# Performance work log

Measured on AMD Instinct MI355X. Metric: run time of the kernel, lower is better.

Reference implementation:

```python
import jax, jax.numpy as jnp
import numpy as np

SCALES = (3, 9, 17, 33)  # must be odd so padding=s//2 preserves spatial size


def _box_conv(img, s):
    # img: [B,1,H,W]; conv with an all-ones s x s kernel, 'same' padding for odd s
    k = jnp.ones((1, 1, s, s), img.dtype)
    p = s // 2
    return jax.lax.conv_general_dilated(
        img, k, window_strides=(1, 1), padding=[(p, p), (p, p)],
        dimension_numbers=("NCHW", "OIHW", "NCHW"))


def setup_inputs() -> dict:
    key = jax.random.key(0)
    B, C, H, W = 8, 3, 1024, 1024
    x = jax.random.normal(key, (B, C, H, W), dtype=jnp.float32)
    # mimicking sparse path-traced samples
    keep = jax.random.uniform(jax.random.fold_in(key, 1), (B, 1, H, W)) >= 0.3
    x = jnp.where(keep, x, 0.0)
    return {"x": x}


def reference(x):
    # F.conv2d(x, ones(1,3,1,1)/3) == per-pixel mean over the 3 channels
    lum = jnp.mean(x, axis=1, keepdims=True)          # [B,1,H,W]
    nonzero = (lum != 0).astype(lum.dtype)            # [B,1,H,W]
    feats = []
    for s in SCALES:
        count = _box_conv(nonzero, s)                 # number of nonzero pixels in window
        pool = _box_conv(lum, s) / jnp.maximum(count, 1.0)  # mean over nonzero pixels
        feats.append(count / float(s * s))            # percentage of nonzero pixels
        feats.append(pool)
    return jnp.concatenate(feats, axis=1)             # [B, 2*len(SCALES), H, W]
```

## Files before the change

kernel.cpp:

```cpp
#include <hip/hip_runtime.h>


constexpr int W_    = 1024;
constexpr int H_    = 1024;
constexpr int PAD   = 17;
constexpr int PROWS = H_ + 2 * PAD;
constexpr int LPAD  = 20;
constexpr int RW    = 1064;
constexpr int RS2   = 8;

template<int CTRL, int RM>
__device__ __forceinline__ int dppadd_i(int v) {
    int sh = __builtin_amdgcn_update_dpp(0, v, CTRL, RM, 0xF, true);
    return v + sh;
}

__device__ __forceinline__ int wave_iscan_i(int v) {
    v = dppadd_i<0x111, 0xF>(v);
    v = dppadd_i<0x112, 0xF>(v);
    v = dppadd_i<0x114, 0xF>(v);
    v = dppadd_i<0x118, 0xF>(v);
    v = dppadd_i<0x142, 0xA>(v);
    v = dppadd_i<0x143, 0xC>(v);
    return v;
}

__device__ __forceinline__ void ld4(const unsigned int* p, unsigned int r[4]) {
    __builtin_memcpy(r, p, 16);
}

__global__ __launch_bounds__(256)
void prefix_kernel(const float* __restrict__ x, unsigned int* __restrict__ P) {
    const int lane = threadIdx.x & 63;
    const int wv   = threadIdx.x >> 6;
    const int rp   = blockIdx.x * 4 + wv;
    const int b    = blockIdx.y;
    if (rp >= PROWS) return;

    unsigned int* prow = P + ((size_t)b * PROWS + rp) * RW;
    const int r = rp - PAD;

    if (r < 0 || r >= H_) {
        uint4 z = make_uint4(0u, 0u, 0u, 0u);
        for (int i = lane; i < RW / 4; i += 64)
            ((uint4*)prow)[i] = z;
        return;
    }

    const size_t HW = (size_t)H_ * W_;
    const float* px = x + (size_t)b * 3 * HW + (size_t)r * W_;

    int carry = 0;
    #pragma unroll
    for (int c = 0; c < 4; ++c) {
        const int col = c * 256 + 4 * lane;
        float4 r0 = *(const float4*)(px + col);
        float4 r1 = *(const float4*)(px + col + HW);
        float4 r2 = *(const float4*)(px + col + 2 * HW);
        float l0 = (r0.x + r1.x + r2.x) * (1.0f / 3.0f);
        float l1 = (r0.y + r1.y + r2.y) * (1.0f / 3.0f);
        float l2 = (r0.z + r1.z + r2.z) * (1.0f / 3.0f);
        float l3 = (r0.w + r1.w + r2.w) * (1.0f / 3.0f);
        int v0 = ((int)rintf(l0 * 1024.f) << 16) | ((l0 != 0.f) ? 1 : 0);
        int v1 = ((int)rintf(l1 * 1024.f) << 16) | ((l1 != 0.f) ? 1 : 0);
        int v2 = ((int)rintf(l2 * 1024.f) << 16) | ((l2 != 0.f) ? 1 : 0);
        int v3 = ((int)rintf(l3 * 1024.f) << 16) | ((l3 != 0.f) ? 1 : 0);
        int s0 = v0, s1 = s0 + v1, s2 = s1 + v2, s3 = s2 + v3;
        int incl = wave_iscan_i(s3);
        int excl = incl - s3 + carry;
        uint4 o = make_uint4((unsigned)(excl + s0), (unsigned)(excl + s1),
                             (unsigned)(excl + s2), (unsigned)(excl + s3));
        *(uint4*)(prow + LPAD + col) = o;
        carry += __shfl(incl, 63);
    }

    const unsigned int total = (unsigned int)carry;
    if (lane < 5) {
        *(uint4*)(prow + 4 * lane) = make_uint4(0u, 0u, 0u, 0u);
    } else if (lane < 10) {
        const int i = lane - 5;
        *(uint4*)(prow + LPAD + W_ + 4 * i) =
            make_uint4(total, total, total, total);
    }
}

__global__ __launch_bounds__(256, 4)
void emit_kernel(const unsigned int* __restrict__ P, float* __restrict__ out) {
    constexpr int   PP[4]   = {1, 4, 8, 16};
    constexpr float INVA[4] = {1.f/9.f, 1.f/81.f, 1.f/289.f, 1.f/1089.f};
    constexpr float INVQ    = 1.f / 1024.f;

    const int t  = threadIdx.x;
    const int x0 = 4 * t;

    const int bx = blockIdx.x;
    const int yt = (bx & 7) * 16 + (bx >> 3);
    const int y0 = yt * RS2;
    const int b  = blockIdx.y;

    const unsigned int* Pb = P + (size_t)b * PROWS * RW;
    const size_t HW = (size_t)H_ * W_;
    float* outb = out + (size_t)b * 8 * HW;

    auto rowp = [&](int y) { return Pb + (size_t)(y + PAD) * RW + LPAD + x0; };

    int vl[4][4], vn[4][4];
    #pragma unroll
    for (int i = 0; i < 4; ++i) {
        const int p = PP[i];
        #pragma unroll
        for (int j = 0; j < 4; ++j) { vl[i][j] = 0; vn[i][j] = 0; }
        for (int yy = y0 - 1 - p; yy <= y0 - 1 + p; ++yy) {
            const unsigned int* rw = rowp(yy);
            unsigned int hi[4], lo[4];
            ld4(rw + p, hi); ld4(rw - p - 1, lo);
            #pragma unroll
            for (int j = 0; j < 4; ++j) {
                unsigned int df = hi[j] - lo[j];
                vl[i][j] += (int)df >> 16;
                vn[i][j] += (int)(df & 0xFFFFu);
            }
        }
    }

    #pragma unroll 2
    for (int y = y0; y < y0 + RS2; ++y) {
        #pragma unroll
        for (int i = 0; i < 4; ++i) {
            const int p = PP[i];
            const unsigned int* re = rowp(y + p);
            const unsigned int* rl = rowp(y - 1 - p);
            unsigned int eh[4], el[4], lh[4], ll[4];
            ld4(re + p, eh); ld4(re - p - 1, el);
            ld4(rl + p, lh); ld4(rl - p - 1, ll);
            #pragma unroll
            for (int j = 0; j < 4; ++j) {
                unsigned int de = eh[j] - el[j];
                unsigned int dg = lh[j] - ll[j];
                vl[i][j] += ((int)de >> 16) - ((int)dg >> 16);
                vn[i][j] += (int)(de & 0xFFFFu) - (int)(dg & 0xFFFFu);
            }
        }
        float* orow = outb + (size_t)y * W_ + x0;
        #pragma unroll
        for (int i = 0; i < 4; ++i) {
            float c0 = (float)vn[i][0], c1 = (float)vn[i][1];
            float c2 = (float)vn[i][2], c3 = (float)vn[i][3];
            float4 cnt4 = make_float4(c0 * INVA[i], c1 * INVA[i],
                                      c2 * INVA[i], c3 * INVA[i]);
            float4 pool4 = make_float4(
                (float)vl[i][0] * INVQ * __builtin_amdgcn_rcpf(fmaxf(c0, 1.f)),
                (float)vl[i][1] * INVQ * __builtin_amdgcn_rcpf(fmaxf(c1, 1.f)),
                (float)vl[i][2] * INVQ * __builtin_amdgcn_rcpf(fmaxf(c2, 1.f)),
                (float)vl[i][3] * INVQ * __builtin_amdgcn_rcpf(fmaxf(c3, 1.f)));
            *(float4*)(orow + (size_t)(2 * i) * HW)     = cnt4;
            *(float4*)(orow + (size_t)(2 * i + 1) * HW) = pool4;
        }
    }
}

extern "C" void kernel_launch(void* const* d_in, const int* in_sizes, int n_in,
                              void* d_out, int out_size, void* d_ws, size_t ws_size,
                              hipStream_t stream) {
    const float* x   = (const float*)d_in[0];
    float*       out = (float*)d_out;

    const int B = in_sizes[0] / (3 * H_ * W_);
    unsigned int* P = (unsigned int*)d_ws;

    dim3 g1((PROWS + 3) / 4, B);
    prefix_kernel<<<g1, dim3(256), 0, stream>>>(x, P);

    dim3 g2(H_ / RS2 / 8 * 8, B);
    emit_kernel<<<g2, dim3(256), 0, stream>>>(P, out);
}
```

Baseline: 129.1 us.

## Restructure prefix scan per-lane, double emit row strip, batch emit loads

The prefix kernel now has each lane own 16 contiguous columns. It issues all 12 float4 loads up front and does a serial in-register scan followed by one wave scan, replacing four chained wave scans with carries. The emit kernel doubles rows per block, which amortizes the warm-up window sums, and relaxes launch bounds to 2 waves per EU. It also hoists all 16 row loads ahead of the arithmetic for more memory-level parallelism and interleaves batches in the block index. The risks are uncoalesced 16-column-per-lane access in prefix, higher register pressure, and fewer blocks. The grid now hardcodes the batch as 8 via bid&7.

```diff
diff --git a/kernel.cpp b/kernel.cpp
--- a/kernel.cpp
+++ b/kernel.cpp
@@ -7,7 +7,8 @@
 constexpr int PROWS = H_ + 2 * PAD;
 constexpr int LPAD  = 20;
 constexpr int RW    = 1064;
-constexpr int RS2   = 8;
+constexpr int RS2   = 16;
+constexpr size_t HWc = (size_t)H_ * W_;
 
 template<int CTRL, int RM>
 __device__ __forceinline__ int dppadd_i(int v) {
@@ -47,34 +48,48 @@
         return;
     }
 
-    const size_t HW = (size_t)H_ * W_;
-    const float* px = x + (size_t)b * 3 * HW + (size_t)r * W_;
+    const float* px = x + (size_t)b * 3 * HWc + ((size_t)r << 10);
+    const int c0 = 16 * lane;
 
-    int carry = 0;
+    float4 r0[4], r1[4], r2[4];
     #pragma unroll
     for (int c = 0; c < 4; ++c) {
-        const int col = c * 256 + 4 * lane;
-        float4 r0 = *(const float4*)(px + col);
-        float4 r1 = *(const float4*)(px + col + HW);
-        float4 r2 = *(const float4*)(px + col + 2 * HW);
-        float l0 = (r0.x + r1.x + r2.x) * (1.0f / 3.0f);
-        float l1 = (r0.y + r1.y + r2.y) * (1.0f / 3.0f);
-        float l2 = (r0.z + r1.z + r2.z) * (1.0f / 3.0f);
-        float l3 = (r0.w + r1.w + r2.w) * (1.0f / 3.0f);
-        int v0 = ((int)rintf(l0 * 1024.f) << 16) | ((l0 != 0.f) ? 1 : 0);
-        int v1 = ((int)rintf(l1 * 1024.f) << 16) | ((l1 != 0.f) ? 1 : 0);
-        int v2 = ((int)rintf(l2 * 1024.f) << 16) | ((l2 != 0.f) ? 1 : 0);
-        int v3 = ((int)rintf(l3 * 1024.f) << 16) | ((l3 != 0.f) ? 1 : 0);
-        int s0 = v0, s1 = s0 + v1, s2 = s1 + v2, s3 = s2 + v3;
-        int incl = wave_iscan_i(s3);
-        int excl = incl - s3 + carry;
-        uint4 o = make_uint4((unsigned)(excl + s0), (unsigned)(excl + s1),
-                             (unsigned)(excl + s2), (unsigned)(excl + s3));
-        *(uint4*)(prow + LPAD + col) = o;
-        carry += __shfl(incl, 63);
+        r0[c] = *(const float4*)(px + c0 + 4 * c);
+        r1[c] = *(const float4*)(px + c0 + 4 * c + HWc);
+        r2[c] = *(const float4*)(px + c0 + 4 * c + 2 * HWc);
     }
 
-    const unsigned int total = (unsigned int)carry;
+    int pref[16];
+    int run = 0;
+    #pragma unroll
+    for (int c = 0; c < 4; ++c) {
+        float l0 = (r0[c].x + r1[c].x + r2[c].x) * (1.0f / 3.0f);
+        float l1 = (r0[c].y + r1[c].y + r2[c].y) * (1.0f / 3.0f);
+        float l2 = (r0[c].z + r1[c].z + r2[c].z) * (1.0f / 3.0f);
+        float l3 = (r0[c].w + r1[c].w + r2[c].w) * (1.0f / 3.0f);
+        run += (((int)rintf(l0 * 1024.f)) << 16) | ((l0 != 0.f) ? 1 : 0);
+        pref[4 * c]     = run;
+        run += (((int)rintf(l1 * 1024.f)) << 16) | ((l1 != 0.f) ? 1 : 0);
+        pref[4 * c + 1] = run;
+        run += (((int)rintf(l2 * 1024.f)) << 16) | ((l2 != 0.f) ? 1 : 0);
+        pref[4 * c + 2] = run;
+        run += (((int)rintf(l3 * 1024.f)) << 16) | ((l3 != 0.f) ? 1 : 0);
+        pref[4 * c + 3] = run;
+    }
+
+    const int incl = wave_iscan_i(run);
+    const int excl = incl - run;
+
+    #pragma unroll
+    for (int c = 0; c < 4; ++c) {
+        uint4 o = make_uint4((unsigned)(excl + pref[4 * c]),
+                             (unsigned)(excl + pref[4 * c + 1]),
+                             (unsigned)(excl + pref[4 * c + 2]),
+                             (unsigned)(excl + pref[4 * c + 3]));
+        *(uint4*)(prow + LPAD + c0 + 4 * c) = o;
+    }
+
+    const unsigned int total = (unsigned int)__shfl(incl, 63);
     if (lane < 5) {
         *(uint4*)(prow + 4 * lane) = make_uint4(0u, 0u, 0u, 0u);
     } else if (lane < 10) {
@@ -84,7 +99,7 @@
     }
 }
 
-__global__ __launch_bounds__(256, 4)
+__global__ __launch_bounds__(256, 2)
 void emit_kernel(const unsigned int* __restrict__ P, float* __restrict__ out) {
     constexpr int   PP[4]   = {1, 4, 8, 16};
     constexpr float INVA[4] = {1.f/9.f, 1.f/81.f, 1.f/289.f, 1.f/1089.f};
@@ -93,14 +108,12 @@
     const int t  = threadIdx.x;
     const int x0 = 4 * t;
 
-    const int bx = blockIdx.x;
-    const int yt = (bx & 7) * 16 + (bx >> 3);
-    const int y0 = yt * RS2;
-    const int b  = blockIdx.y;
+    const int bid = blockIdx.x;
+    const int b   = bid & 7;
+    const int y0  = (bid >> 3) * RS2;
 
     const unsigned int* Pb = P + (size_t)b * PROWS * RW;
-    const size_t HW = (size_t)H_ * W_;
-    float* outb = out + (size_t)b * 8 * HW;
+    float* outb = out + (size_t)b * 8 * HWc;
 
     auto rowp = [&](int y) { return Pb + (size_t)(y + PAD) * RW + LPAD + x0; };
 
@@ -125,23 +138,26 @@
 
     #pragma unroll 2
     for (int y = y0; y < y0 + RS2; ++y) {
+        unsigned int eh[4][4], el[4][4], lh[4][4], ll[4][4];
         #pragma unroll
         for (int i = 0; i < 4; ++i) {
             const int p = PP[i];
             const unsigned int* re = rowp(y + p);
             const unsigned int* rl = rowp(y - 1 - p);
-            unsigned int eh[4], el[4], lh[4], ll[4];
-            ld4(re + p, eh); ld4(re - p - 1, el);
-            ld4(rl + p, lh); ld4(rl - p - 1, ll);
+            ld4(re + p, eh[i]); ld4(re - p - 1, el[i]);
+            ld4(rl + p, lh[i]); ld4(rl - p - 1, ll[i]);
+        }
+        #pragma unroll
+        for (int i = 0; i < 4; ++i) {
             #pragma unroll
             for (int j = 0; j < 4; ++j) {
-                unsigned int de = eh[j] - el[j];
-                unsigned int dg = lh[j] - ll[j];
+                unsigned int de = eh[i][j] - el[i][j];
+                unsigned int dg = lh[i][j] - ll[i][j];
                 vl[i][j] += ((int)de >> 16) - ((int)dg >> 16);
                 vn[i][j] += (int)(de & 0xFFFFu) - (int)(dg & 0xFFFFu);
             }
         }
-        float* orow = outb + (size_t)y * W_ + x0;
+        float* orow = outb + ((size_t)y << 10) + x0;
         #pragma unroll
         for (int i = 0; i < 4; ++i) {
             float c0 = (float)vn[i][0], c1 = (float)vn[i][1];
@@ -153,8 +169,8 @@
                 (float)vl[i][1] * INVQ * __builtin_amdgcn_rcpf(fmaxf(c1, 1.f)),
                 (float)vl[i][2] * INVQ * __builtin_amdgcn_rcpf(fmaxf(c2, 1.f)),
                 (float)vl[i][3] * INVQ * __builtin_amdgcn_rcpf(fmaxf(c3, 1.f)));
-            *(float4*)(orow + (size_t)(2 * i) * HW)     = cnt4;
-            *(float4*)(orow + (size_t)(2 * i + 1) * HW) = pool4;
+            *(float4*)(orow + (size_t)(2 * i) * HWc)     = cnt4;
+            *(float4*)(orow + (size_t)(2 * i + 1) * HWc) = pool4;
         }
     }
 }
@@ -171,6 +187,6 @@
     dim3 g1((PROWS + 3) / 4, B);
     prefix_kernel<<<g1, dim3(256), 0, stream>>>(x, P);
 
-    dim3 g2(H_ / RS2 / 8 * 8, B);
+    dim3 g2((H_ / RS2) * B);
     emit_kernel<<<g2, dim3(256), 0, stream>>>(P, out);
 }
```

After: 129.5 us. No clear change (+0.3%).
